# Kernel optimization log

Measured on AMD Instinct MI355X. Metric: run time of the kernel, lower is better.

The kernel has to match this reference:

```python
import jax, jax.numpy as jnp
import numpy as np

P = 5        # window_size
HEADS = 8
DH = 32      # dim_head
SCALE = DH ** -0.5


def setup_inputs() -> dict:
    key = jax.random.key(0)
    ks = jax.random.split(key, 5)
    b, c, h = 32, 256, 4000
    inner = HEADS * DH  # 256
    x = jax.random.normal(ks[0], (b, c, h), dtype=jnp.float32)
    W_qkv = jax.random.normal(ks[1], (c, inner * 3), dtype=jnp.float32) * (c ** -0.5)
    W_out = jax.random.normal(ks[2], (inner, c), dtype=jnp.float32) * (inner ** -0.5)
    b_out = jax.random.normal(ks[3], (c,), dtype=jnp.float32) * 0.02
    pos_embedding = jax.random.normal(ks[4], (2 * P - 1, 2 * P - 1), dtype=jnp.float32) * 0.02
    return {"x": x, "W_qkv": W_qkv, "W_out": W_out, "b_out": b_out, "pos_embedding": pos_embedding}


def _local_attn(x, W_qkv, W_out, b_out, pos_embedding):
    b, c, h = x.shape
    n = h // P
    # relative-position bias, faithful to torch indexing: rel_index[:,0]=(p-1-a), rel_index[:,1]=(p-a), shape (p,1)
    a = jnp.arange(P)
    bias = pos_embedding[(P - 1 - a)[:, None], (P - a)[:, None]]  # (p, 1)
    mask = jnp.zeros((P, P), x.dtype) + bias                      # (p, p)
    # 'b c (n p) -> (b n) p c'
    xw = x.reshape(b, c, n, P).transpose(0, 2, 3, 1).reshape(b * n, P, c)
    qkv = xw @ W_qkv  # (B, p, 3*inner)
    q, k, v = jnp.split(qkv, 3, axis=-1)
    split_heads = lambda t: t.reshape(b * n, P, HEADS, DH).transpose(0, 2, 1, 3)  # (B, h, p, d)
    q, k, v = split_heads(q), split_heads(k), split_heads(v)
    dots = jnp.einsum('bhid,bhjd->bhij', q, k) * SCALE + mask
    attn = jax.nn.softmax(dots, axis=-1)
    out = jnp.einsum('bhij,bhjd->bhid', attn, v)            # (B, h, p, d)
    out = out.transpose(0, 2, 1, 3).reshape(b * n, P, HEADS * DH)
    out = out @ W_out + b_out                                # (B, p, c_out)
    # '(b n) p c -> b c (n p)'
    out = out.reshape(b, n, P, -1).transpose(0, 3, 1, 2).reshape(b, -1, n * P)
    return out, attn


def reference(x, W_qkv, W_out, b_out, pos_embedding):
    return _local_attn(x, W_qkv, W_out, b_out, pos_embedding)
```

## Files before the change

### kernel.cpp

```cpp
#include <hip/hip_runtime.h>
#include <hip/hip_bf16.h>

typedef __attribute__((ext_vector_type(8))) short short8;
typedef __attribute__((ext_vector_type(4))) float f32x4;

namespace {
constexpr int kC = 256;
constexpr int kH = 4000;
constexpr int kNW = 800;
constexpr int kP = 5;
constexpr int kHeads = 8;
constexpr int kDH = 32;
constexpr float kScale = 0.17677669529663687f;

constexpr int WPB = 8;
constexpr int ROWS = WPB * kP;
constexpr int MT = 3;
constexpr int NTHR = 512;

constexpr int WQKV_PACKED = 3 * 16 * 8 * 64 * 8;
constexpr int WOUT_PACKED = 16 * 8 * 64 * 8;

constexpr int QKV_OFF = 20480;
constexpr int PART_STRIDE = 20480;
constexpr int SM_TOTAL = 81920;
}

__device__ inline float b2f(short s) {
  union { unsigned u; float f; } v;
  v.u = ((unsigned)(unsigned short)s) << 16;
  return v.f;
}
__device__ inline short f2bs(float f) {
  __hip_bfloat16 h = __float2bfloat16(f);
  return *reinterpret_cast<short*>(&h);
}

__global__ void prep_weights(const float* __restrict__ Wqkv,
                             const float* __restrict__ Wout,
                             __hip_bfloat16* __restrict__ wq_p,
                             __hip_bfloat16* __restrict__ wo_p) {
  int idx = blockIdx.x * 256 + threadIdx.x;
  if (idx < WQKV_PACKED) {
    int i = idx & 7;
    int l = (idx >> 3) & 63;
    int kt = (idx >> 9) & 7;
    int nt = (idx >> 12) & 15;
    int part = idx >> 16;
    int k = kt * 32 + (l >> 4) * 8 + i;
    int col = part * 256 + nt * 16 + (l & 15);
    wq_p[idx] = __float2bfloat16(Wqkv[k * 768 + col]);
  }
  if (idx < WOUT_PACKED) {
    int i = idx & 7;
    int l = (idx >> 3) & 63;
    int kt = (idx >> 9) & 7;
    int nt = (idx >> 12) & 15;
    int k = kt * 32 + (l >> 4) * 8 + i;
    int col = nt * 16 + (l & 15);
    wo_p[idx] = __float2bfloat16(Wout[k * 256 + col]);
  }
}

__global__ __launch_bounds__(NTHR, 4) void local_attn_kernel(
    const float* __restrict__ x, const short* __restrict__ wq_p,
    const short* __restrict__ wo_p, const float* __restrict__ b_out,
    float* __restrict__ g_out, float* __restrict__ g_attn) {
  __shared__ __align__(16) char smem[SM_TOTAL];

  const int tid = threadIdx.x;
  const int lane = tid & 63;
  const int wid = tid >> 6;

  const int widx0 = blockIdx.x * WPB;
  const int bi = widx0 / kNW;
  const int h0 = (widx0 % kNW) * kP;

  {
    const float* xb = x + (size_t)bi * kC * kH + h0;
    for (int i = tid; i < kC * ROWS; i += NTHR) {
      int c = i / ROWS, hh = i % ROWS;
      *(__hip_bfloat16*)(smem + hh * 512 + ((c * 2) ^ ((hh & 7) << 4))) =
          __float2bfloat16(xb[c * kH + hh]);
    }
  }
  __syncthreads();

  for (int part = 0; part < 3; ++part) {
    f32x4 acc[MT][2];
#pragma unroll
    for (int m = 0; m < MT; ++m)
#pragma unroll
      for (int n = 0; n < 2; ++n) acc[m][n] = (f32x4){0.f, 0.f, 0.f, 0.f};

#pragma unroll
    for (int kt = 0; kt < 8; ++kt) {
      short8 a[MT];
#pragma unroll
      for (int m = 0; m < MT; ++m) {
        int row = m * 16 + (lane & 15);
        int kb = kt * 64 + ((lane >> 4) << 4);
        a[m] = *(const short8*)(smem + row * 512 + (kb ^ ((row & 7) << 4)));
      }
      short8 b[2];
#pragma unroll
      for (int n = 0; n < 2; ++n) {
        int nt = wid * 2 + n;
        b[n] = *(const short8*)(wq_p +
                                ((((part * 16 + nt) * 8 + kt) * 64 + lane) * 8));
      }
#pragma unroll
      for (int m = 0; m < MT; ++m)
#pragma unroll
        for (int n = 0; n < 2; ++n)
          acc[m][n] = __builtin_amdgcn_mfma_f32_16x16x32_bf16(a[m], b[n],
                                                              acc[m][n], 0, 0, 0);
    }
#pragma unroll
    for (int m = 0; m < MT; ++m)
#pragma unroll
      for (int n = 0; n < 2; ++n)
#pragma unroll
        for (int r = 0; r < 4; ++r) {
          int row = m * 16 + ((lane >> 4) << 2) + r;
          if (row < ROWS) {
            int col = (wid * 2 + n) * 16 + (lane & 15);
            *(__hip_bfloat16*)(smem + QKV_OFF + part * PART_STRIDE + row * 512 +
                               ((col * 2) ^ ((row & 7) << 4))) =
                __float2bfloat16(acc[m][n][r]);
          }
        }
  }
  __syncthreads();

  if (tid < WPB * kHeads * kP) {
    int wl = tid / (kHeads * kP);
    int rem = tid % (kHeads * kP);
    int head = rem / kP, i = rem % kP;
    int qrow = wl * kP + i;
    int qsw = (qrow & 7) << 4;
    const char* qbase = smem + QKV_OFF + qrow * 512;

    float qf[32];
#pragma unroll
    for (int ch = 0; ch < 4; ++ch) {
      short8 v8 = *(const short8*)(qbase + ((head * 64 + ch * 16) ^ qsw));
#pragma unroll
      for (int e = 0; e < 8; ++e) qf[ch * 8 + e] = b2f(v8[e]);
    }

    float dots[kP];
    float mx = -1e30f;
#pragma unroll
    for (int j = 0; j < kP; ++j) {
      int krow = wl * kP + j;
      const char* kbase = smem + QKV_OFF + PART_STRIDE + krow * 512;
      int ksw = (krow & 7) << 4;
      float s = 0.f;
#pragma unroll
      for (int ch = 0; ch < 4; ++ch) {
        short8 kv = *(const short8*)(kbase + ((head * 64 + ch * 16) ^ ksw));
#pragma unroll
        for (int e = 0; e < 8; ++e) s += qf[ch * 8 + e] * b2f(kv[e]);
      }
      s *= kScale;
      dots[j] = s;
      mx = fmaxf(mx, s);
    }
    float sum = 0.f;
#pragma unroll
    for (int j = 0; j < kP; ++j) {
      dots[j] = __expf(dots[j] - mx);
      sum += dots[j];
    }
    float inv = 1.f / sum;

    float* ap = g_attn + (size_t)widx0 * (kHeads * kP * kP) + tid * kP;
#pragma unroll
    for (int j = 0; j < kP; ++j) {
      dots[j] *= inv;
      ap[j] = dots[j];
    }

    float ov[32];
#pragma unroll
    for (int d = 0; d < 32; ++d) ov[d] = 0.f;
#pragma unroll
    for (int j = 0; j < kP; ++j) {
      float aj = dots[j];
      int vrow = wl * kP + j;
      const char* vbase = smem + QKV_OFF + 2 * PART_STRIDE + vrow * 512;
      int vsw = (vrow & 7) << 4;
#pragma unroll
      for (int ch = 0; ch < 4; ++ch) {
        short8 vv = *(const short8*)(vbase + ((head * 64 + ch * 16) ^ vsw));
#pragma unroll
        for (int e = 0; e < 8; ++e) ov[ch * 8 + e] += aj * b2f(vv[e]);
      }
    }
    char* obase = smem + qrow * 512;
#pragma unroll
    for (int ch = 0; ch < 4; ++ch) {
      short8 o8;
#pragma unroll
      for (int e = 0; e < 8; ++e) o8[e] = f2bs(ov[ch * 8 + e]);
      *(short8*)(obase + ((head * 64 + ch * 16) ^ qsw)) = o8;
    }
  }
  __syncthreads();

  f32x4 acc2[MT][2];
#pragma unroll
  for (int m = 0; m < MT; ++m)
#pragma unroll
    for (int n = 0; n < 2; ++n) acc2[m][n] = (f32x4){0.f, 0.f, 0.f, 0.f};

#pragma unroll
  for (int kt = 0; kt < 8; ++kt) {
    short8 a[MT];
#pragma unroll
    for (int m = 0; m < MT; ++m) {
      int row = m * 16 + (lane & 15);
      int kb = kt * 64 + ((lane >> 4) << 4);
      a[m] = *(const short8*)(smem + row * 512 + (kb ^ ((row & 7) << 4)));
    }
    short8 b[2];
#pragma unroll
    for (int n = 0; n < 2; ++n) {
      int nt = wid * 2 + n;
      b[n] = *(const short8*)(wo_p + (((nt * 8 + kt) * 64 + lane) * 8));
    }
#pragma unroll
    for (int m = 0; m < MT; ++m)
#pragma unroll
      for (int n = 0; n < 2; ++n)
        acc2[m][n] = __builtin_amdgcn_mfma_f32_16x16x32_bf16(a[m], b[n],
                                                             acc2[m][n], 0, 0, 0);
  }

  float* outS = (float*)(smem + QKV_OFF);
#pragma unroll
  for (int n = 0; n < 2; ++n) {
    int col = (wid * 2 + n) * 16 + (lane & 15);
    float bias = b_out[col];
#pragma unroll
    for (int m = 0; m < MT; ++m)
#pragma unroll
      for (int r = 0; r < 4; ++r) {
        int row = m * 16 + ((lane >> 4) << 2) + r;
        if (row < ROWS) outS[col * 41 + row] = acc2[m][n][r] + bias;
      }
  }
  __syncthreads();

  {
    float* op = g_out + (size_t)bi * kC * kH + h0;
    for (int i = tid; i < kC * ROWS; i += NTHR) {
      int c = i / ROWS, hh = i % ROWS;
      op[c * kH + hh] = outS[c * 41 + hh];
    }
  }
}

extern "C" void kernel_launch(void* const* d_in, const int* in_sizes, int n_in,
                              void* d_out, int out_size, void* d_ws,
                              size_t ws_size, hipStream_t stream) {
  const float* x = (const float*)d_in[0];
  const float* Wqkv = (const float*)d_in[1];
  const float* Wout = (const float*)d_in[2];
  const float* bout = (const float*)d_in[3];

  short* wq_p = (short*)d_ws;
  short* wo_p = wq_p + WQKV_PACKED;

  prep_weights<<<WQKV_PACKED / 256, 256, 0, stream>>>(
      Wqkv, Wout, (__hip_bfloat16*)wq_p, (__hip_bfloat16*)wo_p);

  float* g_out = (float*)d_out;
  float* g_attn = g_out + (size_t)32 * kC * kH;

  int nblocks = (32 * kNW) / WPB;
  local_attn_kernel<<<nblocks, NTHR, 0, stream>>>(x, wq_p, wo_p, bout, g_out,
                                                  g_attn);
}
```

Measured before the change: 168.9 us.

## Shrink tile to six windows, reuse LDS for QKV, split attention across lane pairs

Each block now handles 6 windows (30 rows, 2 M-tiles) instead of 8, and windows may cross batch boundaries, with tail handling for the last block. The LDS footprint drops from 80KB to 45KB: K and V are computed first, then Q is written over the x buffer after a barrier, and launch bounds are raised to 6 blocks per CU. The attention step uses two threads per (window, head, query), each covering 16 dims, and combines partial dot products with a shuffle. The x load packs two channels per 32-bit LDS store. Smaller tiles waste fewer MFMA rows (30 of 32 instead of 40 of 48) and allow more resident blocks, at the cost of extra barriers and more blocks that each reload the weights.

Measured after the change: 289.6 us. +71.4%, slower.

```diff
diff --git a/kernel.cpp b/kernel.cpp
--- a/kernel.cpp
+++ b/kernel.cpp
@@ -10,20 +10,20 @@
 constexpr int kNW = 800;
 constexpr int kP = 5;
 constexpr int kHeads = 8;
-constexpr int kDH = 32;
 constexpr float kScale = 0.17677669529663687f;
-
-constexpr int WPB = 8;
+constexpr int kTotalWin = 32 * kNW;
+
+constexpr int WPB = 6;
 constexpr int ROWS = WPB * kP;
-constexpr int MT = 3;
+constexpr int MT = 2;
 constexpr int NTHR = 512;
 
 constexpr int WQKV_PACKED = 3 * 16 * 8 * 64 * 8;
 constexpr int WOUT_PACKED = 16 * 8 * 64 * 8;
 
-constexpr int QKV_OFF = 20480;
-constexpr int PART_STRIDE = 20480;
-constexpr int SM_TOTAL = 81920;
+constexpr int RK = 15360;
+constexpr int RV = 30720;
+constexpr int SM_TOTAL = 46080;
 }
 
 __device__ inline float b2f(short s) {
@@ -31,9 +31,9 @@
   v.u = ((unsigned)(unsigned short)s) << 16;
   return v.f;
 }
-__device__ inline short f2bs(float f) {
+__device__ inline unsigned short f2bs(float f) {
   __hip_bfloat16 h = __float2bfloat16(f);
-  return *reinterpret_cast<short*>(&h);
+  return *reinterpret_cast<unsigned short*>(&h);
 }
 
 __global__ void prep_weights(const float* __restrict__ Wqkv,
@@ -62,7 +62,7 @@
   }
 }
 
-__global__ __launch_bounds__(NTHR, 4) void local_attn_kernel(
+__global__ __launch_bounds__(NTHR, 6) void local_attn_kernel(
     const float* __restrict__ x, const short* __restrict__ wq_p,
     const short* __restrict__ wo_p, const float* __restrict__ b_out,
     float* __restrict__ g_out, float* __restrict__ g_attn) {
@@ -73,26 +73,29 @@
   const int wid = tid >> 6;
 
   const int widx0 = blockIdx.x * WPB;
-  const int bi = widx0 / kNW;
-  const int h0 = (widx0 % kNW) * kP;
-
-  {
-    const float* xb = x + (size_t)bi * kC * kH + h0;
-    for (int i = tid; i < kC * ROWS; i += NTHR) {
-      int c = i / ROWS, hh = i % ROWS;
-      *(__hip_bfloat16*)(smem + hh * 512 + ((c * 2) ^ ((hh & 7) << 4))) =
-          __float2bfloat16(xb[c * kH + hh]);
-    }
-  }
-  __syncthreads();
-
-  for (int part = 0; part < 3; ++part) {
+  const int nwin = min(WPB, kTotalWin - widx0);
+  const int nrows = nwin * kP;
+
+  for (int i = tid; i < (kC / 2) * ROWS; i += NTHR) {
+    int cp = i / ROWS, hh = i % ROWS;
+    if (hh < nrows) {
+      int gw = widx0 + hh / kP;
+      int b = gw / kNW;
+      int hl = (gw - b * kNW) * kP + hh % kP;
+      const float* p = x + ((size_t)b * kC + 2 * cp) * kH + hl;
+      unsigned u = (unsigned)f2bs(p[0]) | ((unsigned)f2bs(p[kH]) << 16);
+      *(unsigned*)(smem + hh * 512 + ((cp * 4) ^ ((hh & 7) << 4))) = u;
+    }
+  }
+  __syncthreads();
+
+  for (int pi = 0; pi < 2; ++pi) {
+    const int part = pi + 1;
     f32x4 acc[MT][2];
 #pragma unroll
     for (int m = 0; m < MT; ++m)
 #pragma unroll
       for (int n = 0; n < 2; ++n) acc[m][n] = (f32x4){0.f, 0.f, 0.f, 0.f};
-
 #pragma unroll
     for (int kt = 0; kt < 8; ++kt) {
       short8 a[MT];
@@ -116,6 +119,7 @@
           acc[m][n] = __builtin_amdgcn_mfma_f32_16x16x32_bf16(a[m], b[n],
                                                               acc[m][n], 0, 0, 0);
     }
+    char* dst = smem + part * RK;
 #pragma unroll
     for (int m = 0; m < MT; ++m)
 #pragma unroll
@@ -124,87 +128,135 @@
         for (int r = 0; r < 4; ++r) {
           int row = m * 16 + ((lane >> 4) << 2) + r;
           if (row < ROWS) {
-            int col = (wid * 2 + n) * 16 + (lane & 15);
-            *(__hip_bfloat16*)(smem + QKV_OFF + part * PART_STRIDE + row * 512 +
-                               ((col * 2) ^ ((row & 7) << 4))) =
+            int col = wid * 32 + n * 16 + (lane & 15);
+            *(__hip_bfloat16*)(dst + row * 512 + ((col * 2) ^ ((row & 7) << 4))) =
                 __float2bfloat16(acc[m][n][r]);
           }
         }
   }
-  __syncthreads();
-
-  if (tid < WPB * kHeads * kP) {
-    int wl = tid / (kHeads * kP);
-    int rem = tid % (kHeads * kP);
-    int head = rem / kP, i = rem % kP;
-    int qrow = wl * kP + i;
-    int qsw = (qrow & 7) << 4;
-    const char* qbase = smem + QKV_OFF + qrow * 512;
-
-    float qf[32];
-#pragma unroll
-    for (int ch = 0; ch < 4; ++ch) {
-      short8 v8 = *(const short8*)(qbase + ((head * 64 + ch * 16) ^ qsw));
+  {
+    f32x4 accq[MT][2];
+#pragma unroll
+    for (int m = 0; m < MT; ++m)
+#pragma unroll
+      for (int n = 0; n < 2; ++n) accq[m][n] = (f32x4){0.f, 0.f, 0.f, 0.f};
+#pragma unroll
+    for (int kt = 0; kt < 8; ++kt) {
+      short8 a[MT];
+#pragma unroll
+      for (int m = 0; m < MT; ++m) {
+        int row = m * 16 + (lane & 15);
+        int kb = kt * 64 + ((lane >> 4) << 4);
+        a[m] = *(const short8*)(smem + row * 512 + (kb ^ ((row & 7) << 4)));
+      }
+      short8 b[2];
+#pragma unroll
+      for (int n = 0; n < 2; ++n) {
+        int nt = wid * 2 + n;
+        b[n] = *(const short8*)(wq_p + (((nt * 8 + kt) * 64 + lane) * 8));
+      }
+#pragma unroll
+      for (int m = 0; m < MT; ++m)
+#pragma unroll
+        for (int n = 0; n < 2; ++n)
+          accq[m][n] = __builtin_amdgcn_mfma_f32_16x16x32_bf16(a[m], b[n],
+                                                               accq[m][n], 0, 0, 0);
+    }
+    __syncthreads();
+#pragma unroll
+    for (int m = 0; m < MT; ++m)
+#pragma unroll
+      for (int n = 0; n < 2; ++n)
+#pragma unroll
+        for (int r = 0; r < 4; ++r) {
+          int row = m * 16 + ((lane >> 4) << 2) + r;
+          if (row < ROWS) {
+            int col = wid * 32 + n * 16 + (lane & 15);
+            *(__hip_bfloat16*)(smem + row * 512 + ((col * 2) ^ ((row & 7) << 4))) =
+                __float2bfloat16(accq[m][n][r]);
+          }
+        }
+  }
+  __syncthreads();
+
+  const int task = tid >> 1, half = tid & 1;
+  const bool act = task < nwin * (kHeads * kP);
+  float p5[kP];
+  int qrow = 0, head = 0, wl = 0, cbase = 0, qsw = 0;
+  if (act) {
+    wl = task / (kHeads * kP);
+    int rem = task % (kHeads * kP);
+    head = rem / kP;
+    int i = rem % kP;
+    qrow = wl * kP + i;
+    qsw = (qrow & 7) << 4;
+    cbase = head * 64 + half * 32;
+
+    float qf[16];
+#pragma unroll
+    for (int ch = 0; ch < 2; ++ch) {
+      short8 v8 = *(const short8*)(smem + qrow * 512 + ((cbase + ch * 16) ^ qsw));
 #pragma unroll
       for (int e = 0; e < 8; ++e) qf[ch * 8 + e] = b2f(v8[e]);
     }
-
-    float dots[kP];
     float mx = -1e30f;
 #pragma unroll
     for (int j = 0; j < kP; ++j) {
       int krow = wl * kP + j;
-      const char* kbase = smem + QKV_OFF + PART_STRIDE + krow * 512;
       int ksw = (krow & 7) << 4;
       float s = 0.f;
 #pragma unroll
-      for (int ch = 0; ch < 4; ++ch) {
-        short8 kv = *(const short8*)(kbase + ((head * 64 + ch * 16) ^ ksw));
+      for (int ch = 0; ch < 2; ++ch) {
+        short8 kv =
+            *(const short8*)(smem + RK + krow * 512 + ((cbase + ch * 16) ^ ksw));
 #pragma unroll
         for (int e = 0; e < 8; ++e) s += qf[ch * 8 + e] * b2f(kv[e]);
       }
+      s += __shfl_xor(s, 1);
       s *= kScale;
-      dots[j] = s;
+      p5[j] = s;
       mx = fmaxf(mx, s);
     }
     float sum = 0.f;
 #pragma unroll
     for (int j = 0; j < kP; ++j) {
-      dots[j] = __expf(dots[j] - mx);
-      sum += dots[j];
+      p5[j] = __expf(p5[j] - mx);
+      sum += p5[j];
     }
     float inv = 1.f / sum;
-
-    float* ap = g_attn + (size_t)widx0 * (kHeads * kP * kP) + tid * kP;
+#pragma unroll
+    for (int j = 0; j < kP; ++j) p5[j] *= inv;
+    if (!half) {
+      float* ap = g_attn + (size_t)(widx0 + wl) * 200 + head * 25 + i * 5;
+#pragma unroll
+      for (int j = 0; j < kP; ++j) ap[j] = p5[j];
+    }
+  }
+  __syncthreads();
+
+  if (act) {
+    float ov[16];
+#pragma unroll
+    for (int d = 0; d < 16; ++d) ov[d] = 0.f;
 #pragma unroll
     for (int j = 0; j < kP; ++j) {
-      dots[j] *= inv;
-      ap[j] = dots[j];
-    }
-
-    float ov[32];
-#pragma unroll
-    for (int d = 0; d < 32; ++d) ov[d] = 0.f;
-#pragma unroll
-    for (int j = 0; j < kP; ++j) {
-      float aj = dots[j];
+      float aj = p5[j];
       int vrow = wl * kP + j;
-      const char* vbase = smem + QKV_OFF + 2 * PART_STRIDE + vrow * 512;
       int vsw = (vrow & 7) << 4;
 #pragma unroll
-      for (int ch = 0; ch < 4; ++ch) {
-        short8 vv = *(const short8*)(vbase + ((head * 64 + ch * 16) ^ vsw));
+      for (int ch = 0; ch < 2; ++ch) {
+        short8 vv =
+            *(const short8*)(smem + RV + vrow * 512 + ((cbase + ch * 16) ^ vsw));
 #pragma unroll
         for (int e = 0; e < 8; ++e) ov[ch * 8 + e] += aj * b2f(vv[e]);
       }
     }
-    char* obase = smem + qrow * 512;
-#pragma unroll
-    for (int ch = 0; ch < 4; ++ch) {
+#pragma unroll
+    for (int ch = 0; ch < 2; ++ch) {
       short8 o8;
 #pragma unroll
-      for (int e = 0; e < 8; ++e) o8[e] = f2bs(ov[ch * 8 + e]);
-      *(short8*)(obase + ((head * 64 + ch * 16) ^ qsw)) = o8;
+      for (int e = 0; e < 8; ++e) o8[e] = (short)f2bs(ov[ch * 8 + e]);
+      *(short8*)(smem + qrow * 512 + ((cbase + ch * 16) ^ qsw)) = o8;
     }
   }
   __syncthreads();
@@ -214,7 +266,6 @@
   for (int m = 0; m < MT; ++m)
 #pragma unroll
     for (int n = 0; n < 2; ++n) acc2[m][n] = (f32x4){0.f, 0.f, 0.f, 0.f};
-
 #pragma unroll
   for (int kt = 0; kt < 8; ++kt) {
     short8 a[MT];
@@ -237,27 +288,28 @@
         acc2[m][n] = __builtin_amdgcn_mfma_f32_16x16x32_bf16(a[m], b[n],
                                                              acc2[m][n], 0, 0, 0);
   }
-
-  float* outS = (float*)(smem + QKV_OFF);
+  float* outS = (float*)(smem + RK);
 #pragma unroll
   for (int n = 0; n < 2; ++n) {
-    int col = (wid * 2 + n) * 16 + (lane & 15);
+    int col = wid * 32 + n * 16 + (lane & 15);
     float bias = b_out[col];
 #pragma unroll
     for (int m = 0; m < MT; ++m)
 #pragma unroll
       for (int r = 0; r < 4; ++r) {
         int row = m * 16 + ((lane >> 4) << 2) + r;
-        if (row < ROWS) outS[col * 41 + row] = acc2[m][n][r] + bias;
-      }
-  }
-  __syncthreads();
-
-  {
-    float* op = g_out + (size_t)bi * kC * kH + h0;
-    for (int i = tid; i < kC * ROWS; i += NTHR) {
-      int c = i / ROWS, hh = i % ROWS;
-      op[c * kH + hh] = outS[c * 41 + hh];
+        if (row < ROWS) outS[col * ROWS + row] = acc2[m][n][r] + bias;
+      }
+  }
+  __syncthreads();
+
+  for (int i = tid; i < kC * ROWS; i += NTHR) {
+    int c = i / ROWS, hh = i % ROWS;
+    if (hh < nrows) {
+      int gw = widx0 + hh / kP;
+      int b = gw / kNW;
+      int hl = (gw - b * kNW) * kP + hh % kP;
+      g_out[((size_t)b * kC + c) * kH + hl] = outS[c * ROWS + hh];
     }
   }
 }
@@ -279,7 +331,7 @@
   float* g_out = (float*)d_out;
   float* g_attn = g_out + (size_t)32 * kC * kH;
 
-  int nblocks = (32 * kNW) / WPB;
+  int nblocks = (kTotalWin + WPB - 1) / WPB;
   local_attn_kernel<<<nblocks, NTHR, 0, stream>>>(x, wq_p, wo_p, bout, g_out,
                                                   g_attn);
 }
```
